# Optimization experiments

Measured on AMD Instinct MI355X. Metric: run time of the kernel, lower is better.

The kernel has to match this reference:

```python
import jax, jax.numpy as jnp
import numpy as np

N_ATOM = 4096
NHEADS = 8
C_PER_HEAD = 64
BLOCK_SIZE = 128
LOCAL_WINDOW = 512


def setup_inputs() -> dict:
    key = jax.random.key(0)
    k1, k2, k3, k4 = jax.random.split(key, 4)
    q = jax.random.normal(k1, (N_ATOM, NHEADS, C_PER_HEAD), dtype=jnp.float32)
    k = jax.random.normal(k2, (N_ATOM, NHEADS, C_PER_HEAD), dtype=jnp.float32)
    v = jax.random.normal(k3, (N_ATOM, NHEADS, C_PER_HEAD), dtype=jnp.float32)
    pair_bias = jax.random.normal(k4, (N_ATOM, N_ATOM, NHEADS), dtype=jnp.float32)
    return {"q": q, "k": k, "v": v, "pair_bias": pair_bias}


def reference(q, k, v, pair_bias):
    # Local block-sparse attention: banded blockmask with blocks_per_side
    # = max(1, local_window // block_size) blocks on each side of the diagonal.
    # NOTE: pair_bias is accepted by the original forward but never used
    # (it is not passed to block_sparse_attn_func), so it is ignored here.
    N, H, D = q.shape
    B = BLOCK_SIZE
    bps = max(1, LOCAL_WINDOW // BLOCK_SIZE)  # blocks per side = 4
    nrow = N // B  # N is a multiple of block_size here
    scale = jnp.asarray(D, q.dtype) ** -0.5  # softmax_scale=None -> 1/sqrt(d)

    qb = q.reshape(nrow, B, H, D)
    kb = k.reshape(nrow, B, H, D)
    vb = v.reshape(nrow, B, H, D)

    offs = jnp.arange(-bps, bps + 1)                      # [W], W = 2*bps+1
    cols = jnp.arange(nrow)[:, None] + offs[None, :]      # [nrow, W]
    valid = (cols >= 0) & (cols < nrow)                   # band edge mask
    colsc = jnp.clip(cols, 0, nrow - 1)

    kg = kb[colsc]  # [nrow, W, B, H, D] -- only band blocks gathered
    vg = vb[colsc]

    # scores: [nrow, H, B, W, B]
    scores = jnp.einsum('rihd,rwjhd->rhiwj', qb, kg) * scale
    neg_inf = jnp.asarray(-jnp.inf, scores.dtype)
    scores = jnp.where(valid[:, None, None, :, None], scores, neg_inf)

    p = jax.nn.softmax(scores.reshape(nrow, H, B, -1), axis=-1)
    p = p.reshape(scores.shape)

    out = jnp.einsum('rhiwj,rwjhd->rihd', p, vg)  # [nrow, B, H, D]
    return out.reshape(N, H, D)
```

## Files before the change

kernel.cpp:

```cpp
#include <hip/hip_runtime.h>
#include <hip/hip_bf16.h>

#define NATOM 4096
#define NH 8
#define DIMD 64
#define BLK 128
#define NROW 32
#define BPS 4
#define ROWSTRIDE (NH * DIMD)
#define SCALE 0.125f
#define L2E 1.4426950408889634f

#define TILE_EL (BLK * DIMD)
#define V_LD 136
#define P_LD 136
#define K_LDF 72

#define HEAD_ELEMS (NATOM * DIMD)
#define WS_NEEDED  (2u * NH * HEAD_ELEMS * 2u)

typedef __attribute__((ext_vector_type(8))) short bf16x8;
typedef __attribute__((ext_vector_type(4))) float f32x4;
typedef __attribute__((ext_vector_type(4))) unsigned int u32x4;

__device__ __forceinline__ short f2bf(float x) {
    unsigned int u = __builtin_bit_cast(unsigned int, x);
    unsigned int r = (u + 0x7fffu + ((u >> 16) & 1u)) >> 16;
    return (short)r;
}
__device__ __forceinline__ unsigned int cvtpk(float lo, float hi) {
    unsigned int r;
    asm("v_cvt_pk_bf16_f32 %0, %1, %2" : "=v"(r) : "v"(lo), "v"(hi));
    return r;
}
__device__ __forceinline__ void drain_gll() {
    asm volatile("s_waitcnt vmcnt(0)" ::: "memory");
}

extern "C" __global__ __launch_bounds__(256)
void prep_kernel(const float* __restrict__ k, const float* __restrict__ v,
                 short* __restrict__ Kb, short* __restrict__ Vt)
{
    __shared__ short Tr[DIMD * V_LD];
    const int bid  = blockIdx.x;
    const int h    = bid & 7;
    const int part = bid >> 3;
    const int t    = threadIdx.x;

    if (part < 32) {
        const int nb = part;
        #pragma unroll
        for (int i = 0; i < 4; ++i) {
            int idx = i * 256 + t;
            int row = idx >> 3;
            int c   = idx & 7;
            int d0  = c * 8;
            int grow = nb * BLK + row;
            const float* src = k + (size_t)grow * ROWSTRIDE + h * DIMD + d0;
            float4 a = *(const float4*)src;
            float4 cc = *(const float4*)(src + 4);
            bf16x8 f;
            f[0] = f2bf(a.x); f[1] = f2bf(a.y); f[2] = f2bf(a.z); f[3] = f2bf(a.w);
            f[4] = f2bf(cc.x); f[5] = f2bf(cc.y); f[6] = f2bf(cc.z); f[7] = f2bf(cc.w);
            *(bf16x8*)(Kb + (size_t)h * HEAD_ELEMS + (size_t)grow * DIMD
                       + ((c ^ (grow & 7)) * 8)) = f;
        }
    } else {
        const int nb = part - 32;
        const int vd = t & 63;
        const int g  = t >> 6;
        const float* vp = v + (size_t)(nb * BLK) * ROWSTRIDE + h * DIMD + vd;
        #pragma unroll
        for (int i = 0; i < 8; ++i) {
            int n4 = i * 16 + g * 4;
            const float* vr = vp + (size_t)n4 * ROWSTRIDE;
            short4 s4;
            s4.x = f2bf(vr[0 * ROWSTRIDE]);
            s4.y = f2bf(vr[1 * ROWSTRIDE]);
            s4.z = f2bf(vr[2 * ROWSTRIDE]);
            s4.w = f2bf(vr[3 * ROWSTRIDE]);
            *(short4*)&Tr[vd * V_LD + n4] = s4;
        }
        __syncthreads();
        #pragma unroll
        for (int i = 0; i < 4; ++i) {
            int s  = i * 256 + t;
            int d  = s >> 4;
            int cc = s & 15;
            int kc = cc >> 2;
            int l2 = cc & 3;
            int kA = kc * 32 + l2 * 4;
            short4 a  = *(const short4*)&Tr[d * V_LD + kA];
            short4 c4 = *(const short4*)&Tr[d * V_LD + kA + 16];
            bf16x8 f;
            f[0] = a.x;  f[1] = a.y;  f[2] = a.z;  f[3] = a.w;
            f[4] = c4.x; f[5] = c4.y; f[6] = c4.z; f[7] = c4.w;
            *(bf16x8*)(Vt + (size_t)h * HEAD_ELEMS + (size_t)nb * TILE_EL
                       + d * BLK + ((cc ^ (d & 15)) * 8)) = f;
        }
    }
}

extern "C" __global__ __launch_bounds__(256)
void bsattn_main(const float* __restrict__ q,
                 const short* __restrict__ Kb,
                 const short* __restrict__ Vt,
                 float* __restrict__ out)
{
    __shared__ short Ksh[2][TILE_EL];
    __shared__ short Vsh[2][TILE_EL];

    const int bid = blockIdx.x;
    const int h   = bid & 7;
    const int br  = bid >> 3;
    const int r   = br >> 1;
    const int t   = threadIdx.x;
    const int w   = t >> 6;
    const int lane = t & 63;
    const int lr = lane >> 4;
    const int lc = lane & 15;

    const int qbase = br * 64 + w * 16;
    const float* qp = q + (size_t)(qbase + lc) * ROWSTRIDE + h * DIMD + lr * 8;
    bf16x8 qf[2];
    #pragma unroll
    for (int kc = 0; kc < 2; ++kc) {
        float4 a = *(const float4*)(qp + kc * 32);
        float4 b = *(const float4*)(qp + kc * 32 + 4);
        bf16x8 f;
        f[0] = f2bf(a.x * (SCALE * L2E)); f[1] = f2bf(a.y * (SCALE * L2E));
        f[2] = f2bf(a.z * (SCALE * L2E)); f[3] = f2bf(a.w * (SCALE * L2E));
        f[4] = f2bf(b.x * (SCALE * L2E)); f[5] = f2bf(b.y * (SCALE * L2E));
        f[6] = f2bf(b.z * (SCALE * L2E)); f[7] = f2bf(b.w * (SCALE * L2E));
        qf[kc] = f;
    }
    bf16x8 onesA;
    #pragma unroll
    for (int i = 0; i < 8; ++i) onesA[i] = (short)0x3F80;

    const short* kbase = Kb + (size_t)h * HEAD_ELEMS;
    const short* vbase = Vt + (size_t)h * HEAD_ELEMS;

    f32x4 acc[4] = {};
    f32x4 lacc = {};

    const int kb0 = (r - BPS > 0) ? (r - BPS) : 0;
    const int kb1 = (r + BPS < NROW - 1) ? (r + BPS) : (NROW - 1);

    const short* kt = kbase + (size_t)kb0 * TILE_EL;
    const short* vt = vbase + (size_t)kb0 * TILE_EL;

#define ISSUE(buf, off)                                                           \
    {                                                                             \
        const short* kq = kt + (size_t)(off) * TILE_EL;                           \
        const short* vq = vt + (size_t)(off) * TILE_EL;                           \
        _Pragma("unroll")                                                         \
        for (int i = 0; i < 4; ++i) {                                             \
            int idx = i * 256 + t;                                                \
            __builtin_amdgcn_global_load_lds(                                     \
                (const __attribute__((address_space(1))) unsigned int*)(kq + idx * 8), \
                (__attribute__((address_space(3))) unsigned int*)(&Ksh[buf][idx * 8]), \
                16, 0, 0);                                                        \
            __builtin_amdgcn_global_load_lds(                                     \
                (const __attribute__((address_space(1))) unsigned int*)(vq + idx * 8), \
                (__attribute__((address_space(3))) unsigned int*)(&Vsh[buf][idx * 8]), \
                16, 0, 0);                                                        \
        }                                                                         \
    }

    ISSUE(0, 0);
    if (kb0 < kb1) ISSUE(1, 1);
    drain_gll();
    __syncthreads();

    int cur = 0;
    for (int kb = kb0; kb <= kb1; ++kb) {
        const short* ks = &Ksh[cur][0];
        const short* vs = &Vsh[cur][0];

        f32x4 s[8];
        __builtin_amdgcn_s_setprio(1);
        #pragma unroll
        for (int mt = 0; mt < 8; ++mt) {
            f32x4 z = {};
            int row = mt * 16 + lc;
            #pragma unroll
            for (int kc = 0; kc < 2; ++kc) {
                bf16x8 kf = *(const bf16x8*)&ks[row * DIMD + (((kc * 4 + lr) ^ (row & 7)) * 8)];
                z = __builtin_amdgcn_mfma_f32_16x16x32_bf16(kf, qf[kc], z, 0, 0, 0);
            }
            s[mt] = z;
        }
        __builtin_amdgcn_s_setprio(0);

        #pragma unroll
        for (int mt = 0; mt < 8; ++mt) {
            #pragma unroll
            for (int e = 0; e < 4; ++e)
                s[mt][e] = __builtin_amdgcn_exp2f(s[mt][e]);
        }

        bf16x8 pf[4];
        #pragma unroll
        for (int kc = 0; kc < 4; ++kc) {
            u32x4 pk;
            pk[0] = cvtpk(s[2 * kc][0],     s[2 * kc][1]);
            pk[1] = cvtpk(s[2 * kc][2],     s[2 * kc][3]);
            pk[2] = cvtpk(s[2 * kc + 1][0], s[2 * kc + 1][1]);
            pk[3] = cvtpk(s[2 * kc + 1][2], s[2 * kc + 1][3]);
            pf[kc] = __builtin_bit_cast(bf16x8, pk);
        }

        __builtin_amdgcn_s_setprio(1);
        #pragma unroll
        for (int dn = 0; dn < 4; ++dn) {
            f32x4 o = acc[dn];
            int d = dn * 16 + lc;
            #pragma unroll
            for (int kc = 0; kc < 4; ++kc) {
                bf16x8 vf = *(const bf16x8*)&vs[d * BLK + (((kc * 4 + lr) ^ (d & 15)) * 8)];
                o = __builtin_amdgcn_mfma_f32_16x16x32_bf16(vf, pf[kc], o, 0, 0, 0);
            }
            acc[dn] = o;
        }
        #pragma unroll
        for (int kc = 0; kc < 4; ++kc)
            lacc = __builtin_amdgcn_mfma_f32_16x16x32_bf16(onesA, pf[kc], lacc, 0, 0, 0);
        __builtin_amdgcn_s_setprio(0);

        drain_gll();
        __syncthreads();
        if (kb + 2 <= kb1) ISSUE(cur, kb - kb0 + 2);
        cur ^= 1;
    }

    float inv = 1.0f / lacc[0];
    float* orow = out + (size_t)(qbase + lc) * ROWSTRIDE + h * DIMD;
    #pragma unroll
    for (int dn = 0; dn < 4; ++dn) {
        f32x4 rv;
        rv[0] = acc[dn][0] * inv; rv[1] = acc[dn][1] * inv;
        rv[2] = acc[dn][2] * inv; rv[3] = acc[dn][3] * inv;
        *(float4*)(orow + dn * 16 + lr * 4) = *(float4*)&rv;
    }
#undef ISSUE
}

extern "C" __global__ __launch_bounds__(512)
void bsattn_fallback(const float* __restrict__ q,
                     const float* __restrict__ k,
                     const float* __restrict__ v,
                     float* __restrict__ out)
{
    __shared__ short Ksh[BLK * K_LDF];
    __shared__ short Vsh[DIMD * V_LD];
    __shared__ short Psh[8][16 * P_LD];

    const int r = blockIdx.x;
    const int h = blockIdx.y;
    const int t = threadIdx.x;
    const int w = t >> 6;
    const int lane = t & 63;
    const int lr = lane >> 4;
    const int lc = lane & 15;

    const int krow = t >> 4;
    const int kcol = (t & 15) * 4;
    const int vd  = t & 63;
    const int vkg = t >> 6;

    const int qrow_l = w * 16 + lc;
    const float* qp = q + (size_t)(r * BLK + qrow_l) * ROWSTRIDE + h * DIMD + lr * 8;
    bf16x8 qf[2];
    #pragma unroll
    for (int kc = 0; kc < 2; ++kc) {
        float4 a = *(const float4*)(qp + kc * 32);
        float4 b = *(const float4*)(qp + kc * 32 + 4);
        bf16x8 f;
        f[0] = f2bf(a.x); f[1] = f2bf(a.y); f[2] = f2bf(a.z); f[3] = f2bf(a.w);
        f[4] = f2bf(b.x); f[5] = f2bf(b.y); f[6] = f2bf(b.z); f[7] = f2bf(b.w);
        qf[kc] = f;
    }

    f32x4 acc[4] = {};
    float m_run[4], l_run[4];
    #pragma unroll
    for (int i = 0; i < 4; ++i) { m_run[i] = -1e30f; l_run[i] = 0.0f; }

    const int kb0 = (r - BPS > 0) ? (r - BPS) : 0;
    const int kb1 = (r + BPS < NROW - 1) ? (r + BPS) : (NROW - 1);

    for (int kb = kb0; kb <= kb1; ++kb) {
        __syncthreads();
        const float* kp = k + (size_t)(kb * BLK) * ROWSTRIDE + h * DIMD;
        const float* vp = v + (size_t)(kb * BLK) * ROWSTRIDE + h * DIMD;

        #pragma unroll
        for (int i = 0; i < 4; ++i) {
            float4 kv = *(const float4*)(kp + (size_t)(i * 32 + krow) * ROWSTRIDE + kcol);
            short4 ks;
            ks.x = f2bf(kv.x); ks.y = f2bf(kv.y); ks.z = f2bf(kv.z); ks.w = f2bf(kv.w);
            *(short4*)&Ksh[(i * 32 + krow) * K_LDF + kcol] = ks;

            const float* vr = vp + (size_t)(i * 32 + vkg * 4) * ROWSTRIDE + vd;
            short4 vs;
            vs.x = f2bf(vr[0 * ROWSTRIDE]);
            vs.y = f2bf(vr[1 * ROWSTRIDE]);
            vs.z = f2bf(vr[2 * ROWSTRIDE]);
            vs.w = f2bf(vr[3 * ROWSTRIDE]);
            *(short4*)&Vsh[vd * V_LD + i * 32 + vkg * 4] = vs;
        }
        __syncthreads();

        f32x4 s[8];
        #pragma unroll
        for (int n = 0; n < 8; ++n) {
            f32x4 z = {};
            #pragma unroll
            for (int kc = 0; kc < 2; ++kc) {
                bf16x8 kf = *(const bf16x8*)&Ksh[(n * 16 + lc) * K_LDF + kc * 32 + lr * 8];
                z = __builtin_amdgcn_mfma_f32_16x16x32_bf16(qf[kc], kf, z, 0, 0, 0);
            }
            s[n] = z * SCALE;
        }

        #pragma unroll
        for (int rr = 0; rr < 4; ++rr) {
            float mx = s[0][rr];
            #pragma unroll
            for (int n = 1; n < 8; ++n) mx = fmaxf(mx, s[n][rr]);
            #pragma unroll
            for (int off = 1; off < 16; off <<= 1)
                mx = fmaxf(mx, __shfl_xor(mx, off, 64));
            float mnew = fmaxf(m_run[rr], mx);
            float al = exp2f((m_run[rr] - mnew) * L2E);
            m_run[rr] = mnew;
            float sum = 0.0f;
            #pragma unroll
            for (int n = 0; n < 8; ++n) {
                float p = exp2f((s[n][rr] - mnew) * L2E);
                s[n][rr] = p;
                sum += p;
            }
            #pragma unroll
            for (int off = 1; off < 16; off <<= 1)
                sum += __shfl_xor(sum, off, 64);
            l_run[rr] = l_run[rr] * al + sum;
            #pragma unroll
            for (int dn = 0; dn < 4; ++dn) acc[dn][rr] *= al;
        }

        short* pw = &Psh[w][0];
        #pragma unroll
        for (int n = 0; n < 8; ++n) {
            #pragma unroll
            for (int rr = 0; rr < 4; ++rr) {
                pw[(lr * 4 + rr) * P_LD + n * 16 + lc] = f2bf(s[n][rr]);
            }
        }

        #pragma unroll
        for (int dn = 0; dn < 4; ++dn) {
            f32x4 o = acc[dn];
            #pragma unroll
            for (int kc = 0; kc < 4; ++kc) {
                bf16x8 pfr = *(const bf16x8*)&pw[lc * P_LD + kc * 32 + lr * 8];
                bf16x8 vf = *(const bf16x8*)&Vsh[(dn * 16 + lc) * V_LD + kc * 32 + lr * 8];
                o = __builtin_amdgcn_mfma_f32_16x16x32_bf16(pfr, vf, o, 0, 0, 0);
            }
            acc[dn] = o;
        }
    }

    float* op = out + (size_t)(r * BLK + w * 16) * ROWSTRIDE + h * DIMD;
    #pragma unroll
    for (int rr = 0; rr < 4; ++rr) {
        float inv = 1.0f / l_run[rr];
        float* orow = op + (size_t)(lr * 4 + rr) * ROWSTRIDE;
        #pragma unroll
        for (int dn = 0; dn < 4; ++dn) {
            orow[dn * 16 + lc] = acc[dn][rr] * inv;
        }
    }
}

extern "C" void kernel_launch(void* const* d_in, const int* in_sizes, int n_in,
                              void* d_out, int out_size, void* d_ws, size_t ws_size,
                              hipStream_t stream) {
    const float* q = (const float*)d_in[0];
    const float* k = (const float*)d_in[1];
    const float* v = (const float*)d_in[2];
    float* out = (float*)d_out;

    if (ws_size >= (size_t)WS_NEEDED) {
        short* Kb = (short*)d_ws;
        short* Vt = Kb + (size_t)NH * HEAD_ELEMS;
        prep_kernel<<<512, 256, 0, stream>>>(k, v, Kb, Vt);
        bsattn_main<<<512, 256, 0, stream>>>(q, Kb, Vt, out);
    } else {
        bsattn_fallback<<<dim3(NROW, NH), 512, 0, stream>>>(q, k, v, out);
    }
}
```

Before: 27.09 us.

## Split key/value tiles into 64-row halves to shrink LDS and raise occupancy

Changes the preprocessed V-transpose layout and the main loop so each pipeline stage handles 64 keys instead of 128, halving the shared memory per block and the score registers per iteration. Launch bounds now request 4 blocks per SIMD/CU so more waves can overlap loads with MFMA work. The cost is twice as many loop iterations and barriers per block, plus more frequent global_load_lds issues and drains.

```diff
diff --git a/kernel.cpp b/kernel.cpp
--- a/kernel.cpp
+++ b/kernel.cpp
@@ -11,7 +11,7 @@
 #define SCALE 0.125f
 #define L2E 1.4426950408889634f
 
-#define TILE_EL (BLK * DIMD)
+#define TILE64 (64 * DIMD)
 #define V_LD 136
 #define P_LD 136
 #define K_LDF 72
@@ -84,31 +84,33 @@
         __syncthreads();
         #pragma unroll
         for (int i = 0; i < 4; ++i) {
-            int s  = i * 256 + t;
-            int d  = s >> 4;
-            int cc = s & 15;
-            int kc = cc >> 2;
-            int l2 = cc & 3;
-            int kA = kc * 32 + l2 * 4;
+            int s    = i * 256 + t;
+            int d    = s >> 4;
+            int cc16 = s & 15;
+            int half = cc16 >> 3;
+            int cc   = cc16 & 7;
+            int kc   = cc >> 2;
+            int l2   = cc & 3;
+            int kA   = half * 64 + kc * 32 + l2 * 4;
             short4 a  = *(const short4*)&Tr[d * V_LD + kA];
             short4 c4 = *(const short4*)&Tr[d * V_LD + kA + 16];
             bf16x8 f;
             f[0] = a.x;  f[1] = a.y;  f[2] = a.z;  f[3] = a.w;
             f[4] = c4.x; f[5] = c4.y; f[6] = c4.z; f[7] = c4.w;
-            *(bf16x8*)(Vt + (size_t)h * HEAD_ELEMS + (size_t)nb * TILE_EL
-                       + d * BLK + ((cc ^ (d & 15)) * 8)) = f;
-        }
-    }
-}
-
-extern "C" __global__ __launch_bounds__(256)
+            *(bf16x8*)(Vt + (size_t)h * HEAD_ELEMS + (size_t)(2 * nb + half) * TILE64
+                       + d * 64 + ((cc ^ (d & 7)) * 8)) = f;
+        }
+    }
+}
+
+extern "C" __global__ __launch_bounds__(256, 4)
 void bsattn_main(const float* __restrict__ q,
                  const short* __restrict__ Kb,
                  const short* __restrict__ Vt,
                  float* __restrict__ out)
 {
-    __shared__ short Ksh[2][TILE_EL];
-    __shared__ short Vsh[2][TILE_EL];
+    __shared__ short Ksh[2][TILE64];
+    __shared__ short Vsh[2][TILE64];
 
     const int bid = blockIdx.x;
     const int h   = bid & 7;
@@ -144,18 +146,20 @@
     f32x4 acc[4] = {};
     f32x4 lacc = {};
 
-    const int kb0 = (r - BPS > 0) ? (r - BPS) : 0;
-    const int kb1 = (r + BPS < NROW - 1) ? (r + BPS) : (NROW - 1);
-
-    const short* kt = kbase + (size_t)kb0 * TILE_EL;
-    const short* vt = vbase + (size_t)kb0 * TILE_EL;
+    const int r0 = (r - BPS > 0) ? (r - BPS) : 0;
+    const int r1 = (r + BPS < NROW - 1) ? (r + BPS) : (NROW - 1);
+    const int kb0 = r0 * 2;
+    const int kb1 = r1 * 2 + 1;
+
+    const short* kt = kbase + (size_t)kb0 * TILE64;
+    const short* vt = vbase + (size_t)kb0 * TILE64;
 
 #define ISSUE(buf, off)                                                           \
     {                                                                             \
-        const short* kq = kt + (size_t)(off) * TILE_EL;                           \
-        const short* vq = vt + (size_t)(off) * TILE_EL;                           \
+        const short* kq = kt + (size_t)(off) * TILE64;                            \
+        const short* vq = vt + (size_t)(off) * TILE64;                            \
         _Pragma("unroll")                                                         \
-        for (int i = 0; i < 4; ++i) {                                             \
+        for (int i = 0; i < 2; ++i) {                                             \
             int idx = i * 256 + t;                                                \
             __builtin_amdgcn_global_load_lds(                                     \
                 (const __attribute__((address_space(1))) unsigned int*)(kq + idx * 8), \
@@ -169,7 +173,7 @@
     }
 
     ISSUE(0, 0);
-    if (kb0 < kb1) ISSUE(1, 1);
+    ISSUE(1, 1);
     drain_gll();
     __syncthreads();
 
@@ -178,10 +182,10 @@
         const short* ks = &Ksh[cur][0];
         const short* vs = &Vsh[cur][0];
 
-        f32x4 s[8];
+        f32x4 s[4];
         __builtin_amdgcn_s_setprio(1);
         #pragma unroll
-        for (int mt = 0; mt < 8; ++mt) {
+        for (int mt = 0; mt < 4; ++mt) {
             f32x4 z = {};
             int row = mt * 16 + lc;
             #pragma unroll
@@ -194,15 +198,15 @@
         __builtin_amdgcn_s_setprio(0);
 
         #pragma unroll
-        for (int mt = 0; mt < 8; ++mt) {
+        for (int mt = 0; mt < 4; ++mt) {
             #pragma unroll
             for (int e = 0; e < 4; ++e)
                 s[mt][e] = __builtin_amdgcn_exp2f(s[mt][e]);
         }
 
-        bf16x8 pf[4];
-        #pragma unroll
-        for (int kc = 0; kc < 4; ++kc) {
+        bf16x8 pf[2];
+        #pragma unroll
+        for (int kc = 0; kc < 2; ++kc) {
             u32x4 pk;
             pk[0] = cvtpk(s[2 * kc][0],     s[2 * kc][1]);
             pk[1] = cvtpk(s[2 * kc][2],     s[2 * kc][3]);
@@ -217,14 +221,14 @@
             f32x4 o = acc[dn];
             int d = dn * 16 + lc;
             #pragma unroll
-            for (int kc = 0; kc < 4; ++kc) {
-                bf16x8 vf = *(const bf16x8*)&vs[d * BLK + (((kc * 4 + lr) ^ (d & 15)) * 8)];
+            for (int kc = 0; kc < 2; ++kc) {
+                bf16x8 vf = *(const bf16x8*)&vs[d * 64 + (((kc * 4 + lr) ^ (d & 7)) * 8)];
                 o = __builtin_amdgcn_mfma_f32_16x16x32_bf16(vf, pf[kc], o, 0, 0, 0);
             }
             acc[dn] = o;
         }
         #pragma unroll
-        for (int kc = 0; kc < 4; ++kc)
+        for (int kc = 0; kc < 2; ++kc)
             lacc = __builtin_amdgcn_mfma_f32_16x16x32_bf16(onesA, pf[kc], lacc, 0, 0, 0);
         __builtin_amdgcn_s_setprio(0);
 
```

Result: faster. 26.56 us, median of 2 (-2.0%).

## Split key dimension across waves and reduce partial outputs through shared memory

Applied to the files above, without the earlier changes.

Each wave now processes all 64 query rows of the block against its own 32-key slice of each key tile, instead of 16 query rows against all 128 keys. This cuts per-wave LDS reads of K and V fragments by reusing them across four query groups. Partial outputs and row sums are then summed across waves through a shared-memory reduction that reuses the K/V buffers. In exchange it costs more registers (launch bounds now request 2 blocks per CU), an extra barrier and reduction pass at the end.

```diff
diff --git a/kernel.cpp b/kernel.cpp
--- a/kernel.cpp
+++ b/kernel.cpp
@@ -15,6 +15,7 @@
 #define V_LD 136
 #define P_LD 136
 #define K_LDF 72
+#define RED_ST 68
 
 #define HEAD_ELEMS (NATOM * DIMD)
 #define WS_NEEDED  (2u * NH * HEAD_ELEMS * 2u)
@@ -101,14 +102,17 @@
     }
 }
 
-extern "C" __global__ __launch_bounds__(256)
+extern "C" __global__ __launch_bounds__(256, 2)
 void bsattn_main(const float* __restrict__ q,
                  const short* __restrict__ Kb,
                  const short* __restrict__ Vt,
                  float* __restrict__ out)
 {
-    __shared__ short Ksh[2][TILE_EL];
-    __shared__ short Vsh[2][TILE_EL];
+    __shared__ __align__(16) char SMEM[4 * 64 * RED_ST * 4 + 256 * 4];
+    short* Ksh0 = (short*)SMEM;
+    short* Vsh0 = (short*)(SMEM + 32768);
+    float* Ored = (float*)SMEM;
+    float* Lred = (float*)(SMEM + 4 * 64 * RED_ST * 4);
 
     const int bid = blockIdx.x;
     const int h   = bid & 7;
@@ -120,19 +124,22 @@
     const int lr = lane >> 4;
     const int lc = lane & 15;
 
-    const int qbase = br * 64 + w * 16;
-    const float* qp = q + (size_t)(qbase + lc) * ROWSTRIDE + h * DIMD + lr * 8;
-    bf16x8 qf[2];
-    #pragma unroll
-    for (int kc = 0; kc < 2; ++kc) {
-        float4 a = *(const float4*)(qp + kc * 32);
-        float4 b = *(const float4*)(qp + kc * 32 + 4);
-        bf16x8 f;
-        f[0] = f2bf(a.x * (SCALE * L2E)); f[1] = f2bf(a.y * (SCALE * L2E));
-        f[2] = f2bf(a.z * (SCALE * L2E)); f[3] = f2bf(a.w * (SCALE * L2E));
-        f[4] = f2bf(b.x * (SCALE * L2E)); f[5] = f2bf(b.y * (SCALE * L2E));
-        f[6] = f2bf(b.z * (SCALE * L2E)); f[7] = f2bf(b.w * (SCALE * L2E));
-        qf[kc] = f;
+    const int qbase = br * 64;
+    bf16x8 qf[4][2];
+    #pragma unroll
+    for (int qg = 0; qg < 4; ++qg) {
+        const float* qp = q + (size_t)(qbase + qg * 16 + lc) * ROWSTRIDE + h * DIMD + lr * 8;
+        #pragma unroll
+        for (int kc = 0; kc < 2; ++kc) {
+            float4 a = *(const float4*)(qp + kc * 32);
+            float4 b = *(const float4*)(qp + kc * 32 + 4);
+            bf16x8 f;
+            f[0] = f2bf(a.x * (SCALE * L2E)); f[1] = f2bf(a.y * (SCALE * L2E));
+            f[2] = f2bf(a.z * (SCALE * L2E)); f[3] = f2bf(a.w * (SCALE * L2E));
+            f[4] = f2bf(b.x * (SCALE * L2E)); f[5] = f2bf(b.y * (SCALE * L2E));
+            f[6] = f2bf(b.z * (SCALE * L2E)); f[7] = f2bf(b.w * (SCALE * L2E));
+            qf[qg][kc] = f;
+        }
     }
     bf16x8 onesA;
     #pragma unroll
@@ -141,8 +148,8 @@
     const short* kbase = Kb + (size_t)h * HEAD_ELEMS;
     const short* vbase = Vt + (size_t)h * HEAD_ELEMS;
 
-    f32x4 acc[4] = {};
-    f32x4 lacc = {};
+    f32x4 o[4][4] = {};
+    f32x4 lacc[4] = {};
 
     const int kb0 = (r - BPS > 0) ? (r - BPS) : 0;
     const int kb1 = (r + BPS < NROW - 1) ? (r + BPS) : (NROW - 1);
@@ -159,11 +166,11 @@
             int idx = i * 256 + t;                                                \
             __builtin_amdgcn_global_load_lds(                                     \
                 (const __attribute__((address_space(1))) unsigned int*)(kq + idx * 8), \
-                (__attribute__((address_space(3))) unsigned int*)(&Ksh[buf][idx * 8]), \
+                (__attribute__((address_space(3))) unsigned int*)(Ksh0 + (buf) * TILE_EL + idx * 8), \
                 16, 0, 0);                                                        \
             __builtin_amdgcn_global_load_lds(                                     \
                 (const __attribute__((address_space(1))) unsigned int*)(vq + idx * 8), \
-                (__attribute__((address_space(3))) unsigned int*)(&Vsh[buf][idx * 8]), \
+                (__attribute__((address_space(3))) unsigned int*)(Vsh0 + (buf) * TILE_EL + idx * 8), \
                 16, 0, 0);                                                        \
         }                                                                         \
     }
@@ -175,57 +182,66 @@
 
     int cur = 0;
     for (int kb = kb0; kb <= kb1; ++kb) {
-        const short* ks = &Ksh[cur][0];
-        const short* vs = &Vsh[cur][0];
-
-        f32x4 s[8];
+        const short* ks = Ksh0 + cur * TILE_EL;
+        const short* vs = Vsh0 + cur * TILE_EL;
+
+        bf16x8 kf[2][2];
+        #pragma unroll
+        for (int lm = 0; lm < 2; ++lm) {
+            int row = w * 32 + lm * 16 + lc;
+            #pragma unroll
+            for (int kc = 0; kc < 2; ++kc)
+                kf[lm][kc] = *(const bf16x8*)&ks[row * DIMD + (((kc * 4 + lr) ^ (row & 7)) * 8)];
+        }
+
+        f32x4 s[4][2];
         __builtin_amdgcn_s_setprio(1);
         #pragma unroll
-        for (int mt = 0; mt < 8; ++mt) {
-            f32x4 z = {};
-            int row = mt * 16 + lc;
-            #pragma unroll
-            for (int kc = 0; kc < 2; ++kc) {
-                bf16x8 kf = *(const bf16x8*)&ks[row * DIMD + (((kc * 4 + lr) ^ (row & 7)) * 8)];
-                z = __builtin_amdgcn_mfma_f32_16x16x32_bf16(kf, qf[kc], z, 0, 0, 0);
+        for (int qg = 0; qg < 4; ++qg) {
+            #pragma unroll
+            for (int lm = 0; lm < 2; ++lm) {
+                f32x4 z = {};
+                #pragma unroll
+                for (int kc = 0; kc < 2; ++kc)
+                    z = __builtin_amdgcn_mfma_f32_16x16x32_bf16(kf[lm][kc], qf[qg][kc], z, 0, 0, 0);
+                s[qg][lm] = z;
             }
-            s[mt] = z;
         }
         __builtin_amdgcn_s_setprio(0);
 
         #pragma unroll
-        for (int mt = 0; mt < 8; ++mt) {
-            #pragma unroll
-            for (int e = 0; e < 4; ++e)
-                s[mt][e] = __builtin_amdgcn_exp2f(s[mt][e]);
-        }
+        for (int qg = 0; qg < 4; ++qg)
+            #pragma unroll
+            for (int lm = 0; lm < 2; ++lm)
+                #pragma unroll
+                for (int e = 0; e < 4; ++e)
+                    s[qg][lm][e] = __builtin_amdgcn_exp2f(s[qg][lm][e]);
 
         bf16x8 pf[4];
         #pragma unroll
-        for (int kc = 0; kc < 4; ++kc) {
+        for (int qg = 0; qg < 4; ++qg) {
             u32x4 pk;
-            pk[0] = cvtpk(s[2 * kc][0],     s[2 * kc][1]);
-            pk[1] = cvtpk(s[2 * kc][2],     s[2 * kc][3]);
-            pk[2] = cvtpk(s[2 * kc + 1][0], s[2 * kc + 1][1]);
-            pk[3] = cvtpk(s[2 * kc + 1][2], s[2 * kc + 1][3]);
-            pf[kc] = __builtin_bit_cast(bf16x8, pk);
-        }
-
+            pk[0] = cvtpk(s[qg][0][0], s[qg][0][1]);
+            pk[1] = cvtpk(s[qg][0][2], s[qg][0][3]);
+            pk[2] = cvtpk(s[qg][1][0], s[qg][1][1]);
+            pk[3] = cvtpk(s[qg][1][2], s[qg][1][3]);
+            pf[qg] = __builtin_bit_cast(bf16x8, pk);
+        }
+
+        bf16x8 vf[4];
+        #pragma unroll
+        for (int dn = 0; dn < 4; ++dn) {
+            int d = dn * 16 + lc;
+            vf[dn] = *(const bf16x8*)&vs[d * BLK + (((w * 4 + lr) ^ (d & 15)) * 8)];
+        }
         __builtin_amdgcn_s_setprio(1);
         #pragma unroll
-        for (int dn = 0; dn < 4; ++dn) {
-            f32x4 o = acc[dn];
-            int d = dn * 16 + lc;
-            #pragma unroll
-            for (int kc = 0; kc < 4; ++kc) {
-                bf16x8 vf = *(const bf16x8*)&vs[d * BLK + (((kc * 4 + lr) ^ (d & 15)) * 8)];
-                o = __builtin_amdgcn_mfma_f32_16x16x32_bf16(vf, pf[kc], o, 0, 0, 0);
-            }
-            acc[dn] = o;
-        }
-        #pragma unroll
-        for (int kc = 0; kc < 4; ++kc)
-            lacc = __builtin_amdgcn_mfma_f32_16x16x32_bf16(onesA, pf[kc], lacc, 0, 0, 0);
+        for (int qg = 0; qg < 4; ++qg) {
+            #pragma unroll
+            for (int dn = 0; dn < 4; ++dn)
+                o[qg][dn] = __builtin_amdgcn_mfma_f32_16x16x32_bf16(vf[dn], pf[qg], o[qg][dn], 0, 0, 0);
+            lacc[qg] = __builtin_amdgcn_mfma_f32_16x16x32_bf16(onesA, pf[qg], lacc[qg], 0, 0, 0);
+        }
         __builtin_amdgcn_s_setprio(0);
 
         drain_gll();
@@ -234,14 +250,35 @@
         cur ^= 1;
     }
 
-    float inv = 1.0f / lacc[0];
-    float* orow = out + (size_t)(qbase + lc) * ROWSTRIDE + h * DIMD;
-    #pragma unroll
-    for (int dn = 0; dn < 4; ++dn) {
+    #pragma unroll
+    for (int qg = 0; qg < 4; ++qg) {
+        #pragma unroll
+        for (int dn = 0; dn < 4; ++dn) {
+            *(f32x4*)&Ored[(w * 64 + qg * 16 + lc) * RED_ST + dn * 16 + lr * 4] = o[qg][dn];
+        }
+    }
+    if (lr == 0) {
+        #pragma unroll
+        for (int qg = 0; qg < 4; ++qg)
+            Lred[w * 64 + qg * 16 + lc] = lacc[qg][0];
+    }
+    __syncthreads();
+
+    float l = 0.0f;
+    #pragma unroll
+    for (int wv = 0; wv < 4; ++wv) l += Lred[wv * 64 + w * 16 + lc];
+    float inv = 1.0f / l;
+    float* orow = out + (size_t)(qbase + w * 16 + lc) * ROWSTRIDE + h * DIMD;
+    #pragma unroll
+    for (int e4 = 0; e4 < 4; ++e4) {
+        f32x4 sum = {};
+        #pragma unroll
+        for (int wv = 0; wv < 4; ++wv)
+            sum += *(const f32x4*)&Ored[(wv * 64 + w * 16 + lc) * RED_ST + lr * 16 + e4 * 4];
         f32x4 rv;
-        rv[0] = acc[dn][0] * inv; rv[1] = acc[dn][1] * inv;
-        rv[2] = acc[dn][2] * inv; rv[3] = acc[dn][3] * inv;
-        *(float4*)(orow + dn * 16 + lr * 4) = *(float4*)&rv;
+        rv[0] = sum[0] * inv; rv[1] = sum[1] * inv;
+        rv[2] = sum[2] * inv; rv[3] = sum[3] * inv;
+        *(float4*)(orow + lr * 16 + e4 * 4) = *(float4*)&rv;
     }
 #undef ISSUE
 }
```

Measured after the change: 27.97 us. 3.2% more time.
